# Performance work log

Hardware: AMD Instinct MI355X
Metric: run time of the kernel (lower is better)

## Reference

```python
import jax, jax.numpy as jnp
import numpy as np

# LocalConv config (must match init_kwargs)
B, C, H, W = 64, 16, 64, 64
KH, KW = 3, 3
SH, SW = 1, 1
OUT_CH = 32
OH = (H - KH + SH) // SH  # 62
OW = (W - KW + SW) // SW  # 62
P = OH * OW               # 3844 positions
FEAT = C * KH * KW        # 144 (flatten order: C, kh, kw)


def setup_inputs() -> dict:
    key = jax.random.key(0)
    k1, k2 = jax.random.split(key)
    inputs = jax.random.normal(k1, (B, C, H, W), dtype=jnp.float32)
    kernel = jax.random.normal(k2, (P, FEAT, OUT_CH), dtype=jnp.float32)
    return {"inputs": inputs, "kernel": kernel}


def _extract_patches(x):
    # x: (B, C, H, W) -> (P, B, FEAT) with FEAT flattened as (C, kh, kw),
    # matching torch's reshape of inputs[:, :, i:i+kh, j:j+kw].
    i_idx = (jnp.arange(OH) * SH)[:, None] + jnp.arange(KH)[None, :]  # (OH, KH)
    j_idx = (jnp.arange(OW) * SW)[:, None] + jnp.arange(KW)[None, :]  # (OW, KW)
    # gather -> (B, C, OH, KH, OW, KW)
    p = x[:, :, i_idx[:, :, None, None], j_idx[None, None, :, :]]
    # -> (OH, OW, B, C, KH, KW)
    p = jnp.transpose(p, (2, 4, 0, 1, 3, 5))
    return p.reshape(P, B, FEAT)


def reference(inputs, kernel):
    patches = _extract_patches(inputs)                 # (P, B, FEAT)
    out = jnp.einsum('pbf,pfo->pbo', patches, kernel)  # per-position unshared matmul
    out = out.reshape(OH, OW, B, OUT_CH)
    return jnp.transpose(out, (2, 3, 0, 1))            # (B, OUT_CH, OH, OW)
```

## Files before the change

kernel.cpp:

```cpp
#include <hip/hip_runtime.h>

#define CIN    16
#define HH     64
#define WW     64
#define OHD    62
#define OWD    62
#define OUTC   32
#define FEATN  144
#define POUT   (OHD*OWD)
#define LSTRB  152
#define AR_W   10
#define AR_ELEMS   (3*AR_W*64*16)
#define BBUF_ELEMS (OUTC*LSTRB + 8)
#define SMEM_BYTES ((AR_ELEMS + 2*BBUF_ELEMS)*2)

typedef __attribute__((ext_vector_type(8))) short  short8;
typedef __attribute__((ext_vector_type(4))) float  f32x4;
typedef __attribute__((ext_vector_type(2))) float  f32x2;

__device__ __forceinline__ unsigned short f2bf(float f) {
    unsigned int u = __float_as_uint(f);
    u += 0x7FFFu + ((u >> 16) & 1u);
    return (unsigned short)(u >> 16);
}

template<int TW>
__device__ __forceinline__ void conv_body(
    const float* __restrict__ inp, const float* __restrict__ wgt,
    float* __restrict__ out, int oh, int ow0,
    unsigned short* __restrict__ Araw, unsigned short* __restrict__ B_lds)
{
    const int tid = threadIdx.x;
    constexpr int WTOT = TW + 2;

    for (int t = tid; t < 3 * WTOT * 64; t += 512) {
        int w   = t % WTOT;
        int rem = t / WTOT;
        int b   = rem & 63;
        int kh  = rem >> 6;
        const float* src = inp + (size_t)b * (CIN * HH * WW)
                               + (size_t)(oh + kh) * WW + (ow0 + w);
        short8 h0, h1;
        #pragma unroll
        for (int c = 0; c < 8; ++c) h0[c] = (short)f2bf(src[c * (HH * WW)]);
        #pragma unroll
        for (int c = 0; c < 8; ++c) h1[c] = (short)f2bf(src[(c + 8) * (HH * WW)]);
        int s = (b >> 2) & 1;
        unsigned Gb = (unsigned)(((kh * AR_W + w) * 64 + b) * 2);
        unsigned wx = (unsigned)((w & 3) << 1);
        *(short8*)(Araw + (((Gb + s) ^ wx) << 3))       = h0;
        *(short8*)(Araw + (((Gb + (1 - s)) ^ wx) << 3)) = h1;
    }

    for (int t = tid; t < 2 * 264; t += 512) {
        int buf = t / 264, r = t % 264;
        int e = (r < 256) ? ((r >> 3) * LSTRB + 144 + (r & 7))
                          : (OUTC * LSTRB + (r & 7));
        B_lds[buf * BBUF_ELEMS + e] = 0;
    }

    const int o_w   = tid & 31;
    const int g_w   = (tid >> 6);
    const int h_w   = (tid >> 5) & 1;
    const int gbase  = (h_w * 72 + g_w) * 32 + o_w;
    const int gbase2 = ((((tid >> 5) & 1) * 72 + 8) * 32) + o_w;
    const int woff   = o_w * LSTRB + g_w * 16 + h_w * 8;
    const int woff2  = o_w * LSTRB + 128 + ((tid >> 5) & 1) * 8;
    const int p0 = oh * OWD + ow0;

    float wv[8], wv2[8];
    auto issue = [&](int q) {
        const float* wp = wgt + (size_t)(p0 + q) * (FEATN * OUTC);
        #pragma unroll
        for (int j = 0; j < 8; ++j) wv[j] = wp[gbase + j * 288];
        if (tid < 64) {
            #pragma unroll
            for (int j = 0; j < 8; ++j) wv2[j] = wp[gbase2 + j * 288];
        }
    };
    auto writeB = [&](unsigned short* Bb) {
        short8 sv;
        #pragma unroll
        for (int j = 0; j < 8; ++j) sv[j] = (short)f2bf(wv[j]);
        *(short8*)(Bb + woff) = sv;
        if (tid < 64) {
            short8 sv2;
            #pragma unroll
            for (int j = 0; j < 8; ++j) sv2[j] = (short)f2bf(wv2[j]);
            *(short8*)(Bb + woff2) = sv2;
        }
    };

    const int wid = tid >> 6, lane = tid & 63;
    const int fr = lane & 15, fq = lane >> 4, fqh = fq >> 1;
    const int mt = wid >> 1, nt = wid & 1;
    const int b  = mt * 16 + fr;
    const int gr = (fq & 1) ^ ((b >> 2) & 1);
    unsigned abase_g[5]; int kwv[5]; int boff[5];
    #pragma unroll
    for (int kc = 0; kc < 5; ++kc) {
        int g  = 2 * kc + fqh;
        int gc = (g > 8) ? 8 : g;
        int kh = (gc * 11) >> 5;
        int kw = gc - 3 * kh;
        abase_g[kc] = (unsigned)(((kh * AR_W + kw) * 64 + b) * 2 + gr);
        kwv[kc]     = kw;
        boff[kc]    = (nt * 16 + fr) * LSTRB + kc * 32 + fq * 8;
    }

    issue(0);
    writeB(B_lds);
    issue(1);
    __syncthreads();

    f32x4 acc[TW];
    #pragma unroll
    for (int q = 0; q < TW; ++q) acc[q] = (f32x4){0.f, 0.f, 0.f, 0.f};

    #pragma unroll
    for (int q = 0; q < TW; ++q) {
        const unsigned short* Bc = B_lds + (q & 1) * BBUF_ELEMS;
        #pragma unroll
        for (int kc = 0; kc < 5; ++kc) {
            short8 a;
            if (kc == 4 && fqh == 1) {
                a = (short8){0, 0, 0, 0, 0, 0, 0, 0};
            } else {
                unsigned gi = (abase_g[kc] + (unsigned)(q * 128))
                              ^ (unsigned)(((q + kwv[kc]) & 3) << 1);
                a = *(const short8*)(Araw + (gi << 3));
            }
            short8 bfv = *(const short8*)(Bc + boff[kc]);
            acc[q] = __builtin_amdgcn_mfma_f32_16x16x32_bf16(a, bfv, acc[q], 0, 0, 0);
        }
        if (q + 1 < TW) writeB(B_lds + ((q + 1) & 1) * BBUF_ELEMS);
        __syncthreads();
        if (q + 2 < TW) issue(q + 2);
    }

    const int o = nt * 16 + fr;
    #pragma unroll
    for (int r = 0; r < 4; ++r) {
        float* dst = out + ((size_t)((mt * 16 + fq * 4 + r) * OUTC + o)) * POUT
                         + (size_t)oh * OWD + ow0;
        #pragma unroll
        for (int j = 0; j < TW / 2; ++j) {
            f32x2 v = { acc[2 * j][r], acc[2 * j + 1][r] };
            *(f32x2*)(dst + 2 * j) = v;
        }
    }
}

__global__ __launch_bounds__(512, 4) void localconv_kernel(
    const float* __restrict__ inp,
    const float* __restrict__ wgt,
    float* __restrict__ out)
{
    extern __shared__ unsigned short smem[];
    unsigned short* Araw  = smem;
    unsigned short* B_lds = smem + AR_ELEMS;

    const int l   = (blockIdx.x & 7) * 62 + (blockIdx.x >> 3);
    const int oh  = l >> 3;
    const int owt = l & 7;

    if (owt < 7) conv_body<8>(inp, wgt, out, oh, owt * 8, Araw, B_lds);
    else         conv_body<6>(inp, wgt, out, oh, 56, Araw, B_lds);
}

extern "C" void kernel_launch(void* const* d_in, const int* in_sizes, int n_in,
                              void* d_out, int out_size, void* d_ws, size_t ws_size,
                              hipStream_t stream) {
    const float* inp = (const float*)d_in[0];
    const float* wgt = (const float*)d_in[1];
    float* out = (float*)d_out;
    hipFuncSetAttribute((const void*)localconv_kernel,
                        hipFuncAttributeMaxDynamicSharedMemorySize, SMEM_BYTES);
    localconv_kernel<<<dim3(62 * 8), 512, SMEM_BYTES, stream>>>(inp, wgt, out);
}
```

Before: 37.57 us.

## Use 6-wide strips, 3-deep weight prefetch ring, and XCD-aware block mapping

Each block now covers 6 output columns instead of 8, so the grid grows to 682 blocks (11 strips per row, the last one 2 wide), and the per-block input staging area shrinks. Weight loads are restructured so each thread fetches 9 scalars per position, held in a 3-stage register ring that is issued before the input staging. This puts the loads further ahead of use, and the last iteration's barrier is skipped. Block-to-tile mapping is redone to spread contiguous tiles evenly across the 8 XCDs. In exchange there are more blocks that each re-read overlapping input halos, more register pressure from the ring, and LDS weight writes become scalar 2-byte stores that may bank-conflict.

```diff
diff --git a/kernel.cpp b/kernel.cpp
--- a/kernel.cpp
+++ b/kernel.cpp
@@ -9,7 +9,7 @@
 #define FEATN  144
 #define POUT   (OHD*OWD)
 #define LSTRB  152
-#define AR_W   10
+#define AR_W   8
 #define AR_ELEMS   (3*AR_W*64*16)
 #define BBUF_ELEMS (OUTC*LSTRB + 8)
 #define SMEM_BYTES ((AR_ELEMS + 2*BBUF_ELEMS)*2)
@@ -32,6 +32,27 @@
 {
     const int tid = threadIdx.x;
     constexpr int WTOT = TW + 2;
+
+    const int o_w = tid & 31;
+    const int c_w = tid >> 5;
+    const int p0  = oh * OWD + ow0;
+    const float* wbase = wgt + (size_t)p0 * (FEATN * OUTC) + c_w * 288 + o_w;
+    float ring[3][9];
+    auto issue = [&](int t) {
+        const float* p = wbase + (size_t)t * (FEATN * OUTC);
+        #pragma unroll
+        for (int g = 0; g < 9; ++g) ring[t % 3][g] = p[g * 32];
+    };
+    const int wb_base = o_w * LSTRB + c_w;
+    auto writeB = [&](int t, unsigned short* Bb) {
+        #pragma unroll
+        for (int g = 0; g < 9; ++g)
+            Bb[wb_base + g * 16] = f2bf(ring[t % 3][g]);
+    };
+
+    issue(0);
+    if (1 < TW) issue(1);
+    if (2 < TW) issue(2);
 
     for (int t = tid; t < 3 * WTOT * 64; t += 512) {
         int w   = t % WTOT;
@@ -59,37 +80,7 @@
         B_lds[buf * BBUF_ELEMS + e] = 0;
     }
 
-    const int o_w   = tid & 31;
-    const int g_w   = (tid >> 6);
-    const int h_w   = (tid >> 5) & 1;
-    const int gbase  = (h_w * 72 + g_w) * 32 + o_w;
-    const int gbase2 = ((((tid >> 5) & 1) * 72 + 8) * 32) + o_w;
-    const int woff   = o_w * LSTRB + g_w * 16 + h_w * 8;
-    const int woff2  = o_w * LSTRB + 128 + ((tid >> 5) & 1) * 8;
-    const int p0 = oh * OWD + ow0;
-
-    float wv[8], wv2[8];
-    auto issue = [&](int q) {
-        const float* wp = wgt + (size_t)(p0 + q) * (FEATN * OUTC);
-        #pragma unroll
-        for (int j = 0; j < 8; ++j) wv[j] = wp[gbase + j * 288];
-        if (tid < 64) {
-            #pragma unroll
-            for (int j = 0; j < 8; ++j) wv2[j] = wp[gbase2 + j * 288];
-        }
-    };
-    auto writeB = [&](unsigned short* Bb) {
-        short8 sv;
-        #pragma unroll
-        for (int j = 0; j < 8; ++j) sv[j] = (short)f2bf(wv[j]);
-        *(short8*)(Bb + woff) = sv;
-        if (tid < 64) {
-            short8 sv2;
-            #pragma unroll
-            for (int j = 0; j < 8; ++j) sv2[j] = (short)f2bf(wv2[j]);
-            *(short8*)(Bb + woff2) = sv2;
-        }
-    };
+    writeB(0, B_lds);
 
     const int wid = tid >> 6, lane = tid & 63;
     const int fr = lane & 15, fq = lane >> 4, fqh = fq >> 1;
@@ -108,9 +99,6 @@
         boff[kc]    = (nt * 16 + fr) * LSTRB + kc * 32 + fq * 8;
     }
 
-    issue(0);
-    writeB(B_lds);
-    issue(1);
     __syncthreads();
 
     f32x4 acc[TW];
@@ -133,9 +121,11 @@
             short8 bfv = *(const short8*)(Bc + boff[kc]);
             acc[q] = __builtin_amdgcn_mfma_f32_16x16x32_bf16(a, bfv, acc[q], 0, 0, 0);
         }
-        if (q + 1 < TW) writeB(B_lds + ((q + 1) & 1) * BBUF_ELEMS);
-        __syncthreads();
-        if (q + 2 < TW) issue(q + 2);
+        if (q + 3 < TW) issue(q + 3);
+        if (q + 1 < TW) {
+            writeB(q + 1, B_lds + ((q + 1) & 1) * BBUF_ELEMS);
+            __syncthreads();
+        }
     }
 
     const int o = nt * 16 + fr;
@@ -160,12 +150,14 @@
     unsigned short* Araw  = smem;
     unsigned short* B_lds = smem + AR_ELEMS;
 
-    const int l   = (blockIdx.x & 7) * 62 + (blockIdx.x >> 3);
-    const int oh  = l >> 3;
-    const int owt = l & 7;
+    const int bid = blockIdx.x;
+    const int xcd = bid & 7, i = bid >> 3;
+    const int l   = (xcd < 2) ? xcd * 86 + i : 172 + (xcd - 2) * 85 + i;
+    const int oh    = l / 11;
+    const int strip = l % 11;
 
-    if (owt < 7) conv_body<8>(inp, wgt, out, oh, owt * 8, Araw, B_lds);
-    else         conv_body<6>(inp, wgt, out, oh, 56, Araw, B_lds);
+    if (strip < 10) conv_body<6>(inp, wgt, out, oh, strip * 6, Araw, B_lds);
+    else            conv_body<2>(inp, wgt, out, oh, 60, Araw, B_lds);
 }
 
 extern "C" void kernel_launch(void* const* d_in, const int* in_sizes, int n_in,
@@ -176,5 +168,5 @@
     float* out = (float*)d_out;
     hipFuncSetAttribute((const void*)localconv_kernel,
                         hipFuncAttributeMaxDynamicSharedMemorySize, SMEM_BYTES);
-    localconv_kernel<<<dim3(62 * 8), 512, SMEM_BYTES, stream>>>(inp, wgt, out);
+    localconv_kernel<<<dim3(682), 512, SMEM_BYTES, stream>>>(inp, wgt, out);
 }
```

Measured after the change: 40.50 us. +7.8%, slower.
